# Optimization experiments

Measured on AMD Instinct MI355X. Metric: run time of the kernel, lower is better.

The kernel has to match this reference:

```python
import jax, jax.numpy as jnp
import numpy as np

HIDDEN = 768
MLP_HIDDEN = 3072
HEADS = 12
HEAD_DIM = HIDDEN // HEADS

def setup_inputs() -> dict:
    key = jax.random.key(0)
    ks = jax.random.split(key, 12)
    s = 0.02
    return {
        "x": jax.random.normal(ks[0], (16, 1024, HIDDEN), dtype=jnp.float32),
        "ln1_g": jnp.ones((HIDDEN,), jnp.float32),
        "ln1_b": jnp.zeros((HIDDEN,), jnp.float32),
        "wq": jax.random.normal(ks[1], (HIDDEN, HIDDEN), jnp.float32) * s,
        "wk": jax.random.normal(ks[2], (HIDDEN, HIDDEN), jnp.float32) * s,
        "wv": jax.random.normal(ks[3], (HIDDEN, HIDDEN), jnp.float32) * s,
        "wo": jax.random.normal(ks[4], (HIDDEN, HIDDEN), jnp.float32) * s,
        "bo": jnp.zeros((HIDDEN,), jnp.float32),
        "ln2_g": jnp.ones((HIDDEN,), jnp.float32),
        "ln2_b": jnp.zeros((HIDDEN,), jnp.float32),
        "w1": jax.random.normal(ks[5], (HIDDEN, MLP_HIDDEN), jnp.float32) * s,
        "b1": jnp.zeros((MLP_HIDDEN,), jnp.float32),
        "w2": jax.random.normal(ks[6], (MLP_HIDDEN, HIDDEN), jnp.float32) * s,
        "b2": jnp.zeros((HIDDEN,), jnp.float32),
    }

def _layernorm(x, g, b, eps=1e-5):
    mu = jnp.mean(x, axis=-1, keepdims=True)
    var = jnp.mean(jnp.square(x - mu), axis=-1, keepdims=True)
    return (x - mu) * jax.lax.rsqrt(var + eps) * g + b

def reference(x, ln1_g, ln1_b, wq, wk, wv, wo, bo, ln2_g, ln2_b, w1, b1, w2, b2):
    b, n, _ = x.shape
    h, d = HEADS, HEAD_DIM
    scale = d ** -0.5
    # Attention branch
    xn = _layernorm(x, ln1_g, ln1_b)
    q = (xn @ wq.T).reshape(b, n, h, d).transpose(0, 2, 1, 3)  # bhnd
    k = (xn @ wk.T).reshape(b, n, h, d).transpose(0, 2, 1, 3)
    v = (xn @ wv.T).reshape(b, n, h, d).transpose(0, 2, 1, 3)
    score = jax.nn.softmax(jnp.einsum('bhif,bhjf->bhij', q, k) * scale, axis=-1)
    attn = jnp.einsum('bhij,bhjf->bihf', score, v).reshape(b, n, h * d)
    x = attn @ wo.T + bo + x
    # MLP branch
    xn = _layernorm(x, ln2_g, ln2_b)
    hdn = jax.nn.gelu(xn @ w1 + b1, approximate=False)
    x = hdn @ w2 + b2 + x
    return x
```

## Files before the change

### kernel.cpp

```cpp
#include <hip/hip_runtime.h>
#include <hip/hip_bf16.h>

#define HIDDEN 768
#define MLPH   3072
#define HEADS  12
#define HD     64
#define SEQ    1024
#define BATCH  16
#define MTOT   (BATCH*SEQ)

typedef __attribute__((ext_vector_type(8))) short  short8;
typedef __attribute__((ext_vector_type(4))) short  short4x;
typedef __attribute__((ext_vector_type(8))) __bf16 bf16x8;
typedef __attribute__((ext_vector_type(4))) float  floatx4;

#define CL2 0.18033688011112042f

__device__ inline short f2bf(float f) {
  __hip_bfloat16 h = __float2bfloat16(f);
  return *reinterpret_cast<short*>(&h);
}

__device__ inline floatx4 mfma_bf16(short8 a, short8 b, floatx4 c) {
  return __builtin_amdgcn_mfma_f32_16x16x32_bf16(
      __builtin_bit_cast(bf16x8, a), __builtin_bit_cast(bf16x8, b), c, 0, 0, 0);
}

__device__ inline void gl_lds16(const short* g, short* l) {
  __builtin_amdgcn_global_load_lds(
      (const __attribute__((address_space(1))) unsigned int*)g,
      (__attribute__((address_space(3))) unsigned int*)l, 16, 0, 0);
}

__global__ __launch_bounds__(256) void conv_weights(
    const float* __restrict__ wq, const float* __restrict__ wk,
    const float* __restrict__ wv, const float* __restrict__ wo,
    const float* __restrict__ w1, const float* __restrict__ w2,
    short* __restrict__ wqkvb, short* __restrict__ wob,
    short* __restrict__ w1t,   short* __restrict__ w2t)
{
  int i = blockIdx.x * 256 + threadIdx.x;
  const int HH = HIDDEN * HIDDEN;
  if (i < HH) {
    wqkvb[i]        = f2bf(wq[i]);
    wqkvb[HH + i]   = f2bf(wk[i]);
    wqkvb[2*HH + i] = f2bf(wv[i]);
    wob[i]          = f2bf(wo[i]);
  }
  if (i < HIDDEN * MLPH) {
    int n = i / HIDDEN, k = i % HIDDEN;
    w1t[i] = f2bf(w1[(size_t)k * MLPH + n]);
    int n2 = i / MLPH, k2 = i % MLPH;
    w2t[i] = f2bf(w2[(size_t)k2 * HIDDEN + n2]);
  }
}

__global__ __launch_bounds__(256) void ln_kernel(
    const float* __restrict__ x, const float* __restrict__ g,
    const float* __restrict__ b, short* __restrict__ out)
{
  int row = blockIdx.x;
  const float* xr = x + (size_t)row * HIDDEN;
  int t = threadIdx.x;
  float v0 = xr[t], v1 = xr[t + 256], v2 = xr[t + 512];
  float s  = v0 + v1 + v2;
  float s2 = v0*v0 + v1*v1 + v2*v2;
  for (int off = 32; off > 0; off >>= 1) {
    s  += __shfl_down(s, off);
    s2 += __shfl_down(s2, off);
  }
  __shared__ float red[8];
  __shared__ float stats[2];
  int wave = t >> 6;
  if ((t & 63) == 0) { red[wave] = s; red[4 + wave] = s2; }
  __syncthreads();
  if (t == 0) {
    float S  = red[0] + red[1] + red[2] + red[3];
    float S2 = red[4] + red[5] + red[6] + red[7];
    float mu  = S * (1.0f / HIDDEN);
    float var = S2 * (1.0f / HIDDEN) - mu * mu;
    stats[0] = mu;
    stats[1] = rsqrtf(var + 1e-5f);
  }
  __syncthreads();
  float mu = stats[0], rs = stats[1];
  short* orow = out + (size_t)row * HIDDEN;
  orow[t]       = f2bf((v0 - mu) * rs * g[t]       + b[t]);
  orow[t + 256] = f2bf((v1 - mu) * rs * g[t + 256] + b[t + 256]);
  orow[t + 512] = f2bf((v2 - mu) * rs * g[t + 512] + b[t + 512]);
}

template<int OUTMODE , bool BIAS, bool GELU_E, bool RES,
         bool SCALEQ = false>
__global__ __launch_bounds__(512, 2) void gemm_bt2(
    const short* __restrict__ A, const short* __restrict__ B,
    const float* __restrict__ bias, const float* __restrict__ res,
    void* __restrict__ out, int M, int N, int K)
{
  __shared__ alignas(16) short As[4][8192];
  __shared__ alignas(16) short Bs[4][8192];

  int tid = threadIdx.x;
  int lane = tid & 63, wave = tid >> 6;
  int wr = wave >> 2, wc = wave & 3;
  int quad = lane >> 4, lc = lane & 15;

  int nbx = gridDim.x;
  int nwg = nbx * gridDim.y;
  int orig = blockIdx.y * nbx + blockIdx.x;
  int q8 = nwg >> 3, r8 = nwg & 7;
  int xcd = orig & 7, sub = orig >> 3;
  int wg = (xcd < r8 ? xcd * (q8 + 1) : r8 * (q8 + 1) + (xcd - r8) * q8) + sub;
  int m0 = (wg / nbx) * 256;
  int n0 = (wg % nbx) * 256;

  int srow = tid >> 2;
  int skb  = (tid & 3) ^ ((srow >> 1) & 3);
  const short* ga0 = A + (size_t)(m0 + srow) * K + skb * 8;
  const short* ga1 = ga0 + (size_t)128 * K;
  const short* gb0 = B + (size_t)(n0 + srow) * K + skb * 8;
  const short* gb1 = gb0 + (size_t)128 * K;
  int lbase = wave * 512;

#define STAGE_A(T) {                                        \
    const int _b = (T) & 3;                                 \
    gl_lds16(ga0 + (size_t)(T) * 32, &As[_b][lbase]);       \
    gl_lds16(ga1 + (size_t)(T) * 32, &As[_b][4096 + lbase]);\
  }
#define STAGE_B(T) {                                        \
    const int _b = (T) & 3;                                 \
    gl_lds16(gb0 + (size_t)(T) * 32, &Bs[_b][lbase]);       \
    gl_lds16(gb1 + (size_t)(T) * 32, &Bs[_b][4096 + lbase]);\
  }

  floatx4 acc[8][4];
#pragma unroll
  for (int i = 0; i < 8; ++i)
#pragma unroll
    for (int j = 0; j < 4; ++j) acc[i][j] = floatx4{0.f, 0.f, 0.f, 0.f};

  int apos = (quad ^ ((lc >> 1) & 3)) * 8;
  int arow = wr * 128 + lc;
  int brow = wc * 64 + lc;

  int NT = K >> 5;

  STAGE_A(0); STAGE_B(0); STAGE_A(1); STAGE_B(1); STAGE_A(2); STAGE_B(2);
  asm volatile("s_waitcnt vmcnt(8)" ::: "memory");
  __builtin_amdgcn_s_barrier();
  asm volatile("" ::: "memory");

  for (int t = 0; t < NT; ++t) {
    const short* as_ = As[t & 3];
    const short* bs_ = Bs[t & 3];
    short8 af[8], bfr[4];
    if (t + 3 < NT) STAGE_A(t + 3);
#pragma unroll
    for (int i = 0; i < 4; ++i)
      af[i] = *(const short8*)&as_[(arow + i * 16) * 32 + apos];
#pragma unroll
    for (int j = 0; j < 4; ++j)
      bfr[j] = *(const short8*)&bs_[(brow + j * 16) * 32 + apos];
    __builtin_amdgcn_s_barrier();
    asm volatile("s_waitcnt lgkmcnt(0)" ::: "memory");
    __builtin_amdgcn_sched_barrier(0);
    __builtin_amdgcn_s_setprio(1);
#pragma unroll
    for (int i = 0; i < 4; ++i)
#pragma unroll
      for (int j = 0; j < 4; ++j)
        acc[i][j] = mfma_bf16(af[i], bfr[j], acc[i][j]);
    __builtin_amdgcn_s_setprio(0);
    asm volatile("" ::: "memory");
    if (t + 3 < NT) STAGE_B(t + 3);
#pragma unroll
    for (int i = 4; i < 8; ++i)
      af[i] = *(const short8*)&as_[(arow + i * 16) * 32 + apos];
    __builtin_amdgcn_s_barrier();
    asm volatile("s_waitcnt lgkmcnt(0)" ::: "memory");
    __builtin_amdgcn_sched_barrier(0);
    __builtin_amdgcn_s_setprio(1);
#pragma unroll
    for (int i = 4; i < 8; ++i)
#pragma unroll
      for (int j = 0; j < 4; ++j)
        acc[i][j] = mfma_bf16(af[i], bfr[j], acc[i][j]);
    __builtin_amdgcn_s_setprio(0);
    int ahead = NT - 2 - t;
    if (ahead >= 2)      asm volatile("s_waitcnt vmcnt(8)" ::: "memory");
    else if (ahead == 1) asm volatile("s_waitcnt vmcnt(4)" ::: "memory");
    else if (ahead == 0) asm volatile("s_waitcnt vmcnt(0)" ::: "memory");
    __builtin_amdgcn_s_barrier();
    asm volatile("" ::: "memory");
  }
#undef STAGE_A
#undef STAGE_B

#pragma unroll
  for (int i = 0; i < 8; ++i)
#pragma unroll
    for (int j = 0; j < 4; ++j)
#pragma unroll
      for (int r = 0; r < 4; ++r) {
        int row = m0 + wr * 128 + i * 16 + quad * 4 + r;
        int col = n0 + wc * 64 + j * 16 + lc;
        float v = acc[i][j][r];
        if (BIAS)   v += bias[col];
        if (GELU_E) v = 0.5f * v * (1.0f + erff(v * 0.70710678118f));
        if (RES)    v += res[(size_t)row * N + col];
        if (SCALEQ && col < HIDDEN) v *= CL2;
        if (OUTMODE == 1) ((short*)out)[(size_t)row * N + col] = f2bf(v);
        else              ((float*)out)[(size_t)row * N + col] = v;
      }
}

__global__ __launch_bounds__(256) void vtrans_kernel(
    const short* __restrict__ qkv, short* __restrict__ vtg)
{
  int kt = blockIdx.x, h = blockIdx.y, b = blockIdx.z;
  int t = threadIdx.x;
  __shared__ short Vl[64][72];
  const short* vb = qkv + (size_t)(b * SEQ + kt * 64) * 2304 + 1536 + h * 64;
  int row = t >> 2, seg = t & 3;
  short8 r0 = *(const short8*)(vb + (size_t)row * 2304 + seg * 16);
  short8 r1 = *(const short8*)(vb + (size_t)row * 2304 + seg * 16 + 8);
  *(short8*)&Vl[row][seg * 16]     = r0;
  *(short8*)&Vl[row][seg * 16 + 8] = r1;
  __syncthreads();
  int ks = t >> 7, d = (t & 127) >> 1, hb = t & 1;
  short8 w0;
#pragma unroll
  for (int u = 0; u < 8; ++u) {
    int blk = hb * 2 + (u >> 3), j = u & 7;
    int ksrc = ks * 32 + (blk ^ ((d >> 1) & 3)) * 8 + j;
    w0[u] = Vl[ksrc][d];
  }
  short8 w1;
#pragma unroll
  for (int u = 8; u < 16; ++u) {
    int blk = hb * 2 + (u >> 3), j = u & 7;
    int ksrc = ks * 32 + (blk ^ ((d >> 1) & 3)) * 8 + j;
    w1[u - 8] = Vl[ksrc][d];
  }
  short* o = vtg + ((size_t)((b * HEADS + h) * 16 + kt)) * 4096 + t * 16;
  *(short8*)o       = w0;
  *(short8*)(o + 8) = w1;
}

__global__ __launch_bounds__(512) void attn_kernel(
    const short* __restrict__ qkv, const short* __restrict__ vtg,
    short* __restrict__ out)
{
  int qt = blockIdx.x;
  int h  = blockIdx.y;
  int b  = blockIdx.z;
  int tid = threadIdx.x, lane = tid & 63, wave = tid >> 6;
  int quad = lane >> 4, lc = lane & 15;

  __shared__ alignas(16) short Qs[2 * 128 * 32];
  __shared__ alignas(16) short Ks[2 * 64 * 32];
  __shared__ alignas(16) short Vs[2 * 64 * 32];
  __shared__ alignas(16) short Ps[8][16 * 72];

  const int LDQ = 3 * HIDDEN;
  const short* qb = qkv + (size_t)(b * SEQ) * LDQ + h * HD;
  const short* kb = qb + HIDDEN;
  const short* vt = vtg + (size_t)((b * HEADS + h) * 16) * 4096;

  {
    int row = tid >> 2, blk = tid & 3;
    int kblk = blk ^ ((row >> 1) & 3);
#pragma unroll
    for (int t = 0; t < 2; ++t) {
      const short* g = qb + (size_t)(qt * 128 + row) * LDQ + t * 32 + kblk * 8;
      gl_lds16(g, &Qs[t * 4096 + wave * 512]);
    }
  }
  __syncthreads();

  int pos = quad ^ ((lc >> 1) & 3);
  short8 aq[2];
#pragma unroll
  for (int ks = 0; ks < 2; ++ks)
    aq[ks] = *(const short8*)&Qs[ks * 4096 + (wave * 16 + lc) * 32 + pos * 8];

  floatx4 oacc[4];
#pragma unroll
  for (int n2 = 0; n2 < 4; ++n2) oacc[n2] = floatx4{0.f, 0.f, 0.f, 0.f};
  float lsum = 0.f;

  int srow = (tid >> 2) & 63;
  int sks  = tid >> 8;
  int skb  = (tid & 3) ^ ((srow >> 1) & 3);
  const short* kg0 = kb + (size_t)srow * LDQ + sks * 32 + skb * 8;
  const short* vg0 = vt + tid * 8;
  short* pw = &Ps[wave][0];

  for (int kt = 0; kt < 16; ++kt) {
    gl_lds16(kg0 + (size_t)(kt * 64) * LDQ, &Ks[wave * 512]);
    gl_lds16(vg0 + kt * 4096, &Vs[wave * 512]);
    __syncthreads();

    floatx4 sacc[4];
#pragma unroll
    for (int m2 = 0; m2 < 4; ++m2) sacc[m2] = floatx4{0.f, 0.f, 0.f, 0.f};
#pragma unroll
    for (int ks = 0; ks < 2; ++ks) {
#pragma unroll
      for (int m2 = 0; m2 < 4; ++m2) {
        short8 ak = *(const short8*)&Ks[ks * 2048 + (m2 * 16 + lc) * 32 + pos * 8];
        sacc[m2] = mfma_bf16(ak, aq[ks], sacc[m2]);
      }
    }

#pragma unroll
    for (int m2 = 0; m2 < 4; ++m2) {
      float p0 = exp2f(sacc[m2][0]);
      float p1 = exp2f(sacc[m2][1]);
      float p2 = exp2f(sacc[m2][2]);
      float p3 = exp2f(sacc[m2][3]);
      lsum += (p0 + p1) + (p2 + p3);
      short4x pk;
      pk[0] = f2bf(p0); pk[1] = f2bf(p1); pk[2] = f2bf(p2); pk[3] = f2bf(p3);
      *(short4x*)&pw[lc * 72 + m2 * 16 + quad * 4] = pk;
    }
    asm volatile("s_waitcnt lgkmcnt(0)" ::: "memory");
    __builtin_amdgcn_sched_barrier(0);

#pragma unroll
    for (int ks = 0; ks < 2; ++ks) {
      short8 ap = *(const short8*)&pw[lc * 72 + (ks * 4 + quad) * 8];
#pragma unroll
      for (int n2 = 0; n2 < 4; ++n2) {
        short8 bv = *(const short8*)&Vs[ks * 2048 + (n2 * 16 + lc) * 32 + pos * 8];
        oacc[n2] = mfma_bf16(ap, bv, oacc[n2]);
      }
    }
    __syncthreads();
  }

  float rs = lsum;
  rs += __shfl_xor(rs, 16);
  rs += __shfl_xor(rs, 32);
#pragma unroll
  for (int r = 0; r < 4; ++r) {
    float inv = 1.0f / __shfl(rs, quad * 4 + r);
    int row = b * SEQ + qt * 128 + wave * 16 + quad * 4 + r;
#pragma unroll
    for (int n2 = 0; n2 < 4; ++n2) {
      int col = h * HD + n2 * 16 + lc;
      out[(size_t)row * HIDDEN + col] = f2bf(oacc[n2][r] * inv);
    }
  }
}

extern "C" void kernel_launch(void* const* d_in, const int* in_sizes, int n_in,
                              void* d_out, int out_size, void* d_ws, size_t ws_size,
                              hipStream_t stream) {
  const float* x    = (const float*)d_in[0];
  const float* ln1g = (const float*)d_in[1];
  const float* ln1b = (const float*)d_in[2];
  const float* wq   = (const float*)d_in[3];
  const float* wk   = (const float*)d_in[4];
  const float* wv   = (const float*)d_in[5];
  const float* wo   = (const float*)d_in[6];
  const float* bo   = (const float*)d_in[7];
  const float* ln2g = (const float*)d_in[8];
  const float* ln2b = (const float*)d_in[9];
  const float* w1   = (const float*)d_in[10];
  const float* b1   = (const float*)d_in[11];
  const float* w2   = (const float*)d_in[12];
  const float* b2   = (const float*)d_in[13];

  auto rup = [](size_t b) { return (b + 255) & ~(size_t)255; };
  const size_t wbytes = rup((size_t)3 * HIDDEN * HIDDEN * 2) +
                        rup((size_t)HIDDEN * HIDDEN * 2) +
                        rup((size_t)MLPH * HIDDEN * 2) +
                        rup((size_t)HIDDEN * MLPH * 2);

  int R = SEQ;
  const int cands[4] = {16384, 8192, 4096, 2048};
  for (int i = 0; i < 4; ++i) {
    size_t need = wbytes + rup((size_t)cands[i] * 1536) + rup((size_t)cands[i] * 6144)
                         + rup((size_t)cands[i] * 1536);
    if (need <= ws_size) { R = cands[i]; break; }
  }

  char* ws = (char*)d_ws;
  size_t off = 0;
  auto alloc = [&](size_t bytes) {
    char* p = ws + off;
    off += (bytes + 255) & ~(size_t)255;
    return p;
  };
  short* wqkvb = (short*)alloc((size_t)3 * HIDDEN * HIDDEN * 2);
  short* wob   = (short*)alloc((size_t)HIDDEN * HIDDEN * 2);
  short* w1t   = (short*)alloc((size_t)MLPH * HIDDEN * 2);
  short* w2t   = (short*)alloc((size_t)HIDDEN * MLPH * 2);
  short* slotA = (short*)alloc((size_t)R * 1536);
  short* bigR  = (short*)alloc((size_t)R * 6144);
  short* vtg   = (short*)alloc((size_t)R * 1536);

  conv_weights<<<(HIDDEN * MLPH + 255) / 256, 256, 0, stream>>>(
      wq, wk, wv, wo, w1, w2, wqkvb, wob, w1t, w2t);

  const int nch = MTOT / R;
  for (int c = 0; c < nch; ++c) {
    const float* xc  = x + (size_t)c * R * HIDDEN;
    float*       x2c = (float*)d_out + (size_t)c * R * HIDDEN;

    ln_kernel<<<R, 256, 0, stream>>>(xc, ln1g, ln1b, slotA);
    gemm_bt2<1, false, false, false, true>
        <<<dim3((3 * HIDDEN) / 256, R / 256), 512, 0, stream>>>(
        slotA, wqkvb, nullptr, nullptr, bigR, R, 3 * HIDDEN, HIDDEN);
    vtrans_kernel<<<dim3(16, HEADS, R / SEQ), 256, 0, stream>>>(bigR, vtg);
    attn_kernel<<<dim3(SEQ / 128, HEADS, R / SEQ), 512, 0, stream>>>(
        bigR, vtg, slotA);
    gemm_bt2<0, true, false, true>
        <<<dim3(HIDDEN / 256, R / 256), 512, 0, stream>>>(
        slotA, wob, bo, xc, x2c, R, HIDDEN, HIDDEN);
    ln_kernel<<<R, 256, 0, stream>>>(x2c, ln2g, ln2b, slotA);
    gemm_bt2<1, true, true, false>
        <<<dim3(MLPH / 256, R / 256), 512, 0, stream>>>(
        slotA, w1t, b1, nullptr, bigR, R, MLPH, HIDDEN);
    gemm_bt2<0, true, false, true>
        <<<dim3(HIDDEN / 256, R / 256), 512, 0, stream>>>(
        bigR, w2t, b2, x2c, x2c, R, HIDDEN, MLPH);
  }
}
```

Measured before the change: 658.0 us.

## Restructure GEMM mainloop to double-buffered 64-wide K tiles with finer staging

Replaces the 4-deep ring of 32-wide K tiles in the GEMM with two slots, each holding two 32-wide subtiles, so one loop iteration covers 64 of K. Global-to-LDS loads for the next tile are split into four pieces placed between the four MFMA phases, with adjusted vmcnt waits and barriers. The aim is fewer loop iterations and wait/barrier points per unit of K while keeping loads overlapped with compute. Prefetch distance drops from three tiles of 32 to one tile of 64, which can expose more global-load latency.

```diff
diff --git a/kernel.cpp b/kernel.cpp
--- a/kernel.cpp
+++ b/kernel.cpp
@@ -97,8 +97,8 @@
     const float* __restrict__ bias, const float* __restrict__ res,
     void* __restrict__ out, int M, int N, int K)
 {
-  __shared__ alignas(16) short As[4][8192];
-  __shared__ alignas(16) short Bs[4][8192];
+  __shared__ alignas(16) short As[2][2][8192];
+  __shared__ alignas(16) short Bs[2][2][8192];
 
   int tid = threadIdx.x;
   int lane = tid & 63, wave = tid >> 6;
@@ -116,21 +116,15 @@
 
   int srow = tid >> 2;
   int skb  = (tid & 3) ^ ((srow >> 1) & 3);
-  const short* ga0 = A + (size_t)(m0 + srow) * K + skb * 8;
-  const short* ga1 = ga0 + (size_t)128 * K;
-  const short* gb0 = B + (size_t)(n0 + srow) * K + skb * 8;
-  const short* gb1 = gb0 + (size_t)128 * K;
-  int lbase = wave * 512;
-
-#define STAGE_A(T) {                                        \
-    const int _b = (T) & 3;                                 \
-    gl_lds16(ga0 + (size_t)(T) * 32, &As[_b][lbase]);       \
-    gl_lds16(ga1 + (size_t)(T) * 32, &As[_b][4096 + lbase]);\
-  }
-#define STAGE_B(T) {                                        \
-    const int _b = (T) & 3;                                 \
-    gl_lds16(gb0 + (size_t)(T) * 32, &Bs[_b][lbase]);       \
-    gl_lds16(gb1 + (size_t)(T) * 32, &Bs[_b][4096 + lbase]);\
+  const short* ga = A + (size_t)(m0 + srow) * K + skb * 8;
+  const short* gb = B + (size_t)(n0 + srow) * K + skb * 8;
+  const size_t rowskip = (size_t)128 * K;
+  int lb0 = wave * 512;
+
+#define STAGE_R(MAT, gp, sl, ks, kt) {                         \
+    const short* _g = (gp) + (size_t)(kt) * 64 + (ks) * 32;    \
+    gl_lds16(_g,           &MAT[sl][ks][lb0]);                 \
+    gl_lds16(_g + rowskip, &MAT[sl][ks][4096 + lb0]);          \
   }
 
   floatx4 acc[8][4];
@@ -140,61 +134,81 @@
     for (int j = 0; j < 4; ++j) acc[i][j] = floatx4{0.f, 0.f, 0.f, 0.f};
 
   int apos = (quad ^ ((lc >> 1) & 3)) * 8;
-  int arow = wr * 128 + lc;
-  int brow = wc * 64 + lc;
-
-  int NT = K >> 5;
-
-  STAGE_A(0); STAGE_B(0); STAGE_A(1); STAGE_B(1); STAGE_A(2); STAGE_B(2);
-  asm volatile("s_waitcnt vmcnt(8)" ::: "memory");
-  __builtin_amdgcn_s_barrier();
-  asm volatile("" ::: "memory");
-
-  for (int t = 0; t < NT; ++t) {
-    const short* as_ = As[t & 3];
-    const short* bs_ = Bs[t & 3];
-    short8 af[8], bfr[4];
-    if (t + 3 < NT) STAGE_A(t + 3);
-#pragma unroll
-    for (int i = 0; i < 4; ++i)
-      af[i] = *(const short8*)&as_[(arow + i * 16) * 32 + apos];
-#pragma unroll
-    for (int j = 0; j < 4; ++j)
-      bfr[j] = *(const short8*)&bs_[(brow + j * 16) * 32 + apos];
+#define RD(buf, r) (*(const short8*)&(buf)[(r) * 32 + apos])
+#define MM4x4(IOFF)                                                     \
+    _Pragma("unroll")                                                   \
+    for (int i = 0; i < 4; ++i)                                         \
+      _Pragma("unroll")                                                 \
+      for (int j = 0; j < 4; ++j)                                       \
+        acc[i + IOFF][j] = mfma_bf16(aF[i], bF[j], acc[i + IOFF][j]);
+
+  int NK = K >> 6;
+
+  STAGE_R(As, ga, 0, 0, 0); STAGE_R(Bs, gb, 0, 0, 0);
+  STAGE_R(As, ga, 0, 1, 0); STAGE_R(Bs, gb, 0, 1, 0);
+
+  for (int kt = 0; kt < NK; ++kt) {
+    const int sl = kt & 1;
+    const short (*as_)[8192] = As[sl];
+    const short (*bs_)[8192] = Bs[sl];
+    const int s2 = sl ^ 1;
+    const bool st = (kt + 1 < NK);
+    short8 aF[4], bF[4];
+
+    asm volatile("s_waitcnt vmcnt(2)" ::: "memory");
     __builtin_amdgcn_s_barrier();
+    asm volatile("" ::: "memory");
+#pragma unroll
+    for (int i = 0; i < 4; ++i) aF[i] = RD(as_[0], wr * 128 + i * 16 + lc);
+#pragma unroll
+    for (int j = 0; j < 4; ++j) bF[j] = RD(bs_[0], wc * 64 + j * 16 + lc);
+    if (st) STAGE_R(Bs, gb, s2, 1, kt + 1);
     asm volatile("s_waitcnt lgkmcnt(0)" ::: "memory");
     __builtin_amdgcn_sched_barrier(0);
     __builtin_amdgcn_s_setprio(1);
-#pragma unroll
-    for (int i = 0; i < 4; ++i)
-#pragma unroll
-      for (int j = 0; j < 4; ++j)
-        acc[i][j] = mfma_bf16(af[i], bfr[j], acc[i][j]);
+    MM4x4(0);
     __builtin_amdgcn_s_setprio(0);
+
+    __builtin_amdgcn_s_barrier();
     asm volatile("" ::: "memory");
-    if (t + 3 < NT) STAGE_B(t + 3);
-#pragma unroll
-    for (int i = 4; i < 8; ++i)
-      af[i] = *(const short8*)&as_[(arow + i * 16) * 32 + apos];
-    __builtin_amdgcn_s_barrier();
+#pragma unroll
+    for (int i = 0; i < 4; ++i) aF[i] = RD(as_[0], wr * 128 + (i + 4) * 16 + lc);
+    if (st) STAGE_R(Bs, gb, s2, 0, kt + 1);
     asm volatile("s_waitcnt lgkmcnt(0)" ::: "memory");
     __builtin_amdgcn_sched_barrier(0);
     __builtin_amdgcn_s_setprio(1);
-#pragma unroll
-    for (int i = 4; i < 8; ++i)
-#pragma unroll
-      for (int j = 0; j < 4; ++j)
-        acc[i][j] = mfma_bf16(af[i], bfr[j], acc[i][j]);
+    MM4x4(4);
     __builtin_amdgcn_s_setprio(0);
-    int ahead = NT - 2 - t;
-    if (ahead >= 2)      asm volatile("s_waitcnt vmcnt(8)" ::: "memory");
-    else if (ahead == 1) asm volatile("s_waitcnt vmcnt(4)" ::: "memory");
-    else if (ahead == 0) asm volatile("s_waitcnt vmcnt(0)" ::: "memory");
+
+    if (st) asm volatile("s_waitcnt vmcnt(4)" ::: "memory");
+    else    asm volatile("s_waitcnt vmcnt(0)" ::: "memory");
     __builtin_amdgcn_s_barrier();
     asm volatile("" ::: "memory");
-  }
-#undef STAGE_A
-#undef STAGE_B
+#pragma unroll
+    for (int i = 0; i < 4; ++i) aF[i] = RD(as_[1], wr * 128 + i * 16 + lc);
+#pragma unroll
+    for (int j = 0; j < 4; ++j) bF[j] = RD(bs_[1], wc * 64 + j * 16 + lc);
+    if (st) STAGE_R(As, ga, s2, 0, kt + 1);
+    asm volatile("s_waitcnt lgkmcnt(0)" ::: "memory");
+    __builtin_amdgcn_sched_barrier(0);
+    __builtin_amdgcn_s_setprio(1);
+    MM4x4(0);
+    __builtin_amdgcn_s_setprio(0);
+
+    __builtin_amdgcn_s_barrier();
+    asm volatile("" ::: "memory");
+#pragma unroll
+    for (int i = 0; i < 4; ++i) aF[i] = RD(as_[1], wr * 128 + (i + 4) * 16 + lc);
+    if (st) STAGE_R(As, ga, s2, 1, kt + 1);
+    asm volatile("s_waitcnt lgkmcnt(0)" ::: "memory");
+    __builtin_amdgcn_sched_barrier(0);
+    __builtin_amdgcn_s_setprio(1);
+    MM4x4(4);
+    __builtin_amdgcn_s_setprio(0);
+  }
+#undef STAGE_R
+#undef RD
+#undef MM4x4
 
 #pragma unroll
   for (int i = 0; i < 8; ++i)
```

Result: faster. 598.9 us (-9.0%).
